# Kernel tuning notes

Measured on AMD Instinct MI355X. Metric: run time of the kernel, lower is better.

The kernel has to match this reference:

```python
import jax, jax.numpy as jnp
import numpy as np

E = 16        # extra_first_dim / num_experts
N = 32768     # total tokens (sum of num_inputs_per_group)
D = 2048      # input_dim
O = 2048      # output_dim


def setup_inputs() -> dict:
    key = jax.random.key(0)
    k1, k2 = jax.random.split(key)
    x = jax.random.normal(k1, (N, D), dtype=jnp.float32)
    weight = jax.random.normal(k2, (E, D, O), dtype=jnp.float32) * (1.0 / np.sqrt(D))
    # contiguous, equal-size groups summing to N (2048 tokens per expert)
    num_inputs_per_group = jnp.full((E,), N // E, dtype=jnp.int32)
    return {"x": x, "weight": weight, "num_inputs_per_group": num_inputs_per_group}


def reference(x, weight, num_inputs_per_group):
    # Grouped GEMM: rows of x are contiguous per group; row i uses weight[seg[i]].
    # seg: (N,) expert id per token, derived from group sizes (matches torch cumsum slicing).
    n_groups = weight.shape[0]
    n_tokens = x.shape[0]
    seg = jnp.repeat(jnp.arange(n_groups, dtype=jnp.int32), num_inputs_per_group,
                     total_repeat_length=n_tokens)

    def step(acc, ew):
        e, w = ew  # w: (D, O)
        xe = jnp.where((seg == e)[:, None], x, jnp.zeros((), x.dtype))  # mask rows of this group
        return acc + xe @ w, None

    init = jnp.zeros((n_tokens, weight.shape[2]), dtype=x.dtype)
    out, _ = jax.lax.scan(step, init, (jnp.arange(n_groups, dtype=jnp.int32), weight))
    # gang.size == 1: scatter_input / reduce_output are identities.
    return out
```

## Files before the change

### kernel.cpp

```cpp
#include <hip/hip_runtime.h>
#include <hip/hip_bf16.h>
#include <stdint.h>

#define N_TOK 32768
#define DIM   2048
#define ODIM  2048
#define NEXP  16

#define BM 256
#define BN 256
#define BK 64
#define NT (DIM / BK)

#define GLOBAL_AS __attribute__((address_space(1)))
#define LDS_AS    __attribute__((address_space(3)))

typedef short bf8_t  __attribute__((ext_vector_type(8)));
typedef float f4_t   __attribute__((ext_vector_type(4)));

__device__ __forceinline__ uint16_t f32_to_bf16_rne(float f) {
    uint32_t u = __float_as_uint(f);
    uint32_t r = (u + 0x7FFFu + ((u >> 16) & 1u)) >> 16;
    return (uint16_t)r;
}

__global__ void cvt_x_kernel(const float* __restrict__ x,
                             uint16_t* __restrict__ xb, int n4) {
    int i = blockIdx.x * blockDim.x + threadIdx.x;
    if (i >= n4) return;
    float4 v = ((const float4*)x)[i];
    ushort4 o;
    o.x = f32_to_bf16_rne(v.x);
    o.y = f32_to_bf16_rne(v.y);
    o.z = f32_to_bf16_rne(v.z);
    o.w = f32_to_bf16_rne(v.w);
    ((ushort4*)xb)[i] = o;
}

__global__ void cvt_wT_kernel(const float* __restrict__ w,
                              uint16_t* __restrict__ wT) {
    __shared__ float s[64][65];
    const int e  = blockIdx.z;
    const int o0 = blockIdx.x * 64;
    const int d0 = blockIdx.y * 64;
    const float*  we  = w  + (size_t)e * DIM * ODIM;
    uint16_t*     wTe = wT + (size_t)e * (size_t)ODIM * DIM;
    const int c  = threadIdx.x & 63;
    const int r0 = threadIdx.x >> 6;
#pragma unroll
    for (int r = r0; r < 64; r += 4)
        s[r][c] = we[(size_t)(d0 + r) * ODIM + (o0 + c)];
    __syncthreads();
#pragma unroll
    for (int r = r0; r < 64; r += 4)
        wTe[(size_t)(o0 + r) * DIM + (d0 + c)] = f32_to_bf16_rne(s[c][r]);
}

__device__ __forceinline__ void async_copy16(const uint16_t* g, uint16_t* l) {
    __builtin_amdgcn_global_load_lds((const GLOBAL_AS void*)g,
                                     (LDS_AS void*)l, 16, 0, 0);
}

#define STAGE_A(BUF, HALF, KT) do {                                           \
    const uint16_t* _g = aSrc + (size_t)(HALF) * 128 * DIM + (KT) * 64;       \
    uint16_t* _l = aDst + (BUF) * 16384 + (HALF) * 8192;                      \
    async_copy16(_g, _l);                                                     \
    async_copy16(_g + (size_t)64 * DIM, _l + 4096);                           \
} while (0)

#define STAGE_B(BUF, HALF, KT) do {                                           \
    const uint16_t* _g = bSrc + (size_t)(HALF) * 128 * DIM + (KT) * 64;       \
    uint16_t* _l = bDst + (BUF) * 16384 + (HALF) * 8192;                      \
    async_copy16(_g, _l);                                                     \
    async_copy16(_g + (size_t)64 * DIM, _l + 4096);                           \
} while (0)

#define PHASE(BUF, MH, NH, STAGE_CODE, TAIL_CODE) do {                        \
    bf8_t af[4][2], bf[2][2];                                                 \
    const uint16_t* _a = Afr + (BUF) * 16384 + (MH) * 8192;                   \
    const uint16_t* _b = Bfr + (BUF) * 16384 + (NH) * 8192;                   \
    _Pragma("unroll") for (int mi = 0; mi < 4; ++mi)                          \
        _Pragma("unroll") for (int ks = 0; ks < 2; ++ks)                      \
            af[mi][ks] = *(const bf8_t*)(_a + mi * 1024 + ks * 32);           \
    _Pragma("unroll") for (int ni = 0; ni < 2; ++ni)                          \
        _Pragma("unroll") for (int ks = 0; ks < 2; ++ks)                      \
            bf[ni][ks] = *(const bf8_t*)(_b + ni * 1024 + ks * 32);           \
    STAGE_CODE                                                                \
    __builtin_amdgcn_s_barrier();                                             \
    asm volatile("s_waitcnt lgkmcnt(0)" ::: "memory");                        \
    __builtin_amdgcn_sched_barrier(0);                                        \
    __builtin_amdgcn_s_setprio(1);                                            \
    _Pragma("unroll") for (int ks = 0; ks < 2; ++ks)                          \
        _Pragma("unroll") for (int mi = 0; mi < 4; ++mi)                      \
            _Pragma("unroll") for (int ni = 0; ni < 2; ++ni)                  \
                acc[MH][NH][mi][ni] = __builtin_amdgcn_mfma_f32_16x16x32_bf16(\
                    af[mi][ks], bf[ni][ks], acc[MH][NH][mi][ni], 0, 0, 0);    \
    __builtin_amdgcn_s_setprio(0);                                            \
    TAIL_CODE                                                                 \
    __builtin_amdgcn_s_barrier();                                             \
} while (0)

__global__ void __launch_bounds__(512, 2)
grouped_gemm_kernel(const uint16_t* __restrict__ A,
                    const uint16_t* __restrict__ BT,
                    const int* __restrict__ gsize,
                    float* __restrict__ C) {
    __shared__ __align__(16) uint16_t smem[65536];

    const int bid = blockIdx.x;
    const int wg  = (bid & 7) * 128 + (bid >> 3);
    const int tile_m = wg >> 3;
    const int tile_n = wg & 7;
    const int row0 = tile_m * BM;
    const int col0 = tile_n * BN;

    int e = 0, base = 0;
#pragma unroll
    for (int i = 0; i < NEXP; ++i) {
        int nx = base + gsize[i];
        if (row0 >= nx) { base = nx; e = i + 1; }
    }
    const uint16_t* Be = BT + (size_t)e * (size_t)ODIM * DIM;

    const int tid  = threadIdx.x;
    const int lane = tid & 63;
    const int wave = tid >> 6;
    const int wm   = wave >> 2;
    const int wn   = wave & 3;
    const int fr   = lane & 15;
    const int fq   = lane >> 4;

    const int d0   = wave * 1024 + lane * 16;
    const int l0   = d0 ^ (((d0 >> 9) & 1) << 5);
    const int srow = l0 >> 7;
    const int scol = (l0 & 127) >> 1;
    const uint16_t* aSrc = A  + (size_t)(row0 + srow) * DIM + scol;
    const uint16_t* bSrc = Be + (size_t)(col0 + srow) * DIM + scol;
    uint16_t* const aDst = smem + wave * 512;
    uint16_t* const bDst = smem + 32768 + wave * 512;

    const int xorel = ((fr >> 2) & 1) << 4;
    const uint16_t* const Afr = smem + (size_t)(wm * 64 + fr) * 64
                                     + ((fq * 8) ^ xorel);
    const uint16_t* const Bfr = smem + 32768 + (size_t)(wn * 32 + fr) * 64
                                     + ((fq * 8) ^ xorel);

    f4_t acc[2][2][4][2] = {};

    STAGE_A(0, 0, 0); STAGE_A(0, 1, 0); STAGE_B(0, 0, 0); STAGE_B(0, 1, 0);
    STAGE_A(1, 0, 1); STAGE_B(1, 0, 1);
    asm volatile("s_waitcnt vmcnt(4)" ::: "memory");
    __builtin_amdgcn_s_barrier();

#pragma unroll 1
    for (int j = 0; j < NT; j += 2) {
        PHASE(0, 0, 0, { STAGE_A(1, 1, j + 1); STAGE_B(1, 1, j + 1); }, {});
        PHASE(0, 0, 1, {}, {});
        PHASE(0, 1, 0, { if (j + 2 < NT) STAGE_A(0, 0, j + 2); }, {});
        PHASE(0, 1, 1, { if (j + 2 < NT) STAGE_B(0, 0, j + 2); },
              { if (j + 2 < NT) asm volatile("s_waitcnt vmcnt(4)" ::: "memory");
                else            asm volatile("s_waitcnt vmcnt(0)" ::: "memory"); });
        PHASE(1, 0, 0, { if (j + 2 < NT) { STAGE_A(0, 1, j + 2); STAGE_B(0, 1, j + 2); } }, {});
        PHASE(1, 0, 1, {}, {});
        PHASE(1, 1, 0, { if (j + 3 < NT) STAGE_A(1, 0, j + 3); }, {});
        PHASE(1, 1, 1, { if (j + 3 < NT) STAGE_B(1, 0, j + 3); },
              { if (j + 3 < NT) asm volatile("s_waitcnt vmcnt(4)" ::: "memory");
                else            asm volatile("s_waitcnt vmcnt(0)" ::: "memory"); });
    }

    float* Cb = C + (size_t)(row0 + wm * 64 + fq * 4) * ODIM
                  + (col0 + wn * 32 + fr);
#pragma unroll
    for (int mh = 0; mh < 2; ++mh)
#pragma unroll
        for (int nh = 0; nh < 2; ++nh)
#pragma unroll
            for (int mi = 0; mi < 4; ++mi)
#pragma unroll
                for (int ni = 0; ni < 2; ++ni)
#pragma unroll
                    for (int r = 0; r < 4; ++r)
                        Cb[(size_t)(mh * 128 + mi * 16 + r) * ODIM
                           + nh * 128 + ni * 16] = acc[mh][nh][mi][ni][r];
}

extern "C" void kernel_launch(void* const* d_in, const int* in_sizes, int n_in,
                              void* d_out, int out_size, void* d_ws, size_t ws_size,
                              hipStream_t stream) {
    const float* x  = (const float*)d_in[0];
    const float* w  = (const float*)d_in[1];
    const int*   gs = (const int*)d_in[2];
    float* out = (float*)d_out;

    uint16_t* xb = (uint16_t*)d_ws;
    uint16_t* wT = xb + (size_t)N_TOK * DIM;

    int n4 = N_TOK * DIM / 4;
    cvt_x_kernel<<<(n4 + 255) / 256, 256, 0, stream>>>(x, xb, n4);

    dim3 tg(ODIM / 64, DIM / 64, NEXP);
    cvt_wT_kernel<<<tg, 256, 0, stream>>>(w, wT);

    grouped_gemm_kernel<<<dim3((ODIM / BN) * (N_TOK / BM)), 512, 0, stream>>>(
        xb, wT, gs, out);
}
```

Before: 948.6 us.

## Vectorize conversion kernels, reuse LDS fragments across phases, widen LDS swizzle

```diff
diff --git a/kernel.cpp b/kernel.cpp
--- a/kernel.cpp
+++ b/kernel.cpp
@@ -17,6 +17,7 @@
 
 typedef short bf8_t  __attribute__((ext_vector_type(8)));
 typedef float f4_t   __attribute__((ext_vector_type(4)));
+typedef unsigned short us8_t __attribute__((ext_vector_type(8)));
 
 __device__ __forceinline__ uint16_t f32_to_bf16_rne(float f) {
     uint32_t u = __float_as_uint(f);
@@ -25,16 +26,18 @@
 }
 
 __global__ void cvt_x_kernel(const float* __restrict__ x,
-                             uint16_t* __restrict__ xb, int n4) {
-    int i = blockIdx.x * blockDim.x + threadIdx.x;
-    if (i >= n4) return;
-    float4 v = ((const float4*)x)[i];
-    ushort4 o;
-    o.x = f32_to_bf16_rne(v.x);
-    o.y = f32_to_bf16_rne(v.y);
-    o.z = f32_to_bf16_rne(v.z);
-    o.w = f32_to_bf16_rne(v.w);
-    ((ushort4*)xb)[i] = o;
+                             uint16_t* __restrict__ xb, int n8) {
+    const int stride = gridDim.x * blockDim.x;
+    for (int i = blockIdx.x * blockDim.x + threadIdx.x; i < n8; i += stride) {
+        float4 a = ((const float4*)x)[2 * i];
+        float4 b = ((const float4*)x)[2 * i + 1];
+        us8_t o;
+        o[0] = f32_to_bf16_rne(a.x); o[1] = f32_to_bf16_rne(a.y);
+        o[2] = f32_to_bf16_rne(a.z); o[3] = f32_to_bf16_rne(a.w);
+        o[4] = f32_to_bf16_rne(b.x); o[5] = f32_to_bf16_rne(b.y);
+        o[6] = f32_to_bf16_rne(b.z); o[7] = f32_to_bf16_rne(b.w);
+        ((us8_t*)xb)[i] = o;
+    }
 }
 
 __global__ void cvt_wT_kernel(const float* __restrict__ w,
@@ -45,15 +48,24 @@
     const int d0 = blockIdx.y * 64;
     const float*  we  = w  + (size_t)e * DIM * ODIM;
     uint16_t*     wTe = wT + (size_t)e * (size_t)ODIM * DIM;
-    const int c  = threadIdx.x & 63;
-    const int r0 = threadIdx.x >> 6;
-#pragma unroll
-    for (int r = r0; r < 64; r += 4)
-        s[r][c] = we[(size_t)(d0 + r) * ODIM + (o0 + c)];
+    const int tid = threadIdx.x;
+    const int c4  = (tid & 15) * 4;
+    const int r0  = tid >> 4;
+#pragma unroll
+    for (int r = r0; r < 64; r += 16)
+        *(float4*)&s[r][c4] =
+            *(const float4*)&we[(size_t)(d0 + r) * ODIM + o0 + c4];
     __syncthreads();
-#pragma unroll
-    for (int r = r0; r < 64; r += 4)
-        wTe[(size_t)(o0 + r) * DIM + (d0 + c)] = f32_to_bf16_rne(s[c][r]);
+    const int g   = tid & 7;
+    const int or0 = tid >> 3;
+#pragma unroll
+    for (int oo = or0; oo < 64; oo += 32) {
+        us8_t v;
+#pragma unroll
+        for (int j = 0; j < 8; ++j)
+            v[j] = f32_to_bf16_rne(s[g * 8 + j][oo]);
+        *(us8_t*)&wTe[(size_t)(o0 + oo) * DIM + d0 + g * 8] = v;
+    }
 }
 
 __device__ __forceinline__ void async_copy16(const uint16_t* g, uint16_t* l) {
@@ -75,16 +87,25 @@
     async_copy16(_g + (size_t)64 * DIM, _l + 4096);                           \
 } while (0)
 
-#define PHASE(BUF, MH, NH, STAGE_CODE, TAIL_CODE) do {                        \
-    bf8_t af[4][2], bf[2][2];                                                 \
-    const uint16_t* _a = Afr + (BUF) * 16384 + (MH) * 8192;                   \
-    const uint16_t* _b = Bfr + (BUF) * 16384 + (NH) * 8192;                   \
-    _Pragma("unroll") for (int mi = 0; mi < 4; ++mi)                          \
-        _Pragma("unroll") for (int ks = 0; ks < 2; ++ks)                      \
-            af[mi][ks] = *(const bf8_t*)(_a + mi * 1024 + ks * 32);           \
-    _Pragma("unroll") for (int ni = 0; ni < 2; ++ni)                          \
-        _Pragma("unroll") for (int ks = 0; ks < 2; ++ks)                      \
-            bf[ni][ks] = *(const bf8_t*)(_b + ni * 1024 + ks * 32);           \
+#define LOAD_A(dst, BUF, MH) do {                                             \
+    const uint16_t* _p = smem + (BUF) * 16384 + (MH) * 8192;                  \
+    _Pragma("unroll") for (int mi = 0; mi < 4; ++mi) {                        \
+        const uint16_t* _r = _p + (wm * 64 + mi * 16 + fr) * 64;              \
+        dst[mi][0] = *(const bf8_t*)(_r + colk0);                             \
+        dst[mi][1] = *(const bf8_t*)(_r + colk1);                             \
+    }                                                                         \
+} while (0)
+
+#define LOAD_B(dst, BUF, NH) do {                                             \
+    const uint16_t* _p = smem + 32768 + (BUF) * 16384 + (NH) * 8192;          \
+    _Pragma("unroll") for (int ni = 0; ni < 2; ++ni) {                        \
+        const uint16_t* _r = _p + (wn * 32 + ni * 16 + fr) * 64;              \
+        dst[ni][0] = *(const bf8_t*)(_r + colk0);                             \
+        dst[ni][1] = *(const bf8_t*)(_r + colk1);                             \
+    }                                                                         \
+} while (0)
+
+#define PHASE_CORE(AF, BF, MH, NH, STAGE_CODE, TAIL_CODE) do {                \
     STAGE_CODE                                                                \
     __builtin_amdgcn_s_barrier();                                             \
     asm volatile("s_waitcnt lgkmcnt(0)" ::: "memory");                        \
@@ -94,7 +115,7 @@
         _Pragma("unroll") for (int mi = 0; mi < 4; ++mi)                      \
             _Pragma("unroll") for (int ni = 0; ni < 2; ++ni)                  \
                 acc[MH][NH][mi][ni] = __builtin_amdgcn_mfma_f32_16x16x32_bf16(\
-                    af[mi][ks], bf[ni][ks], acc[MH][NH][mi][ni], 0, 0, 0);    \
+                    AF[mi][ks], BF[ni][ks], acc[MH][NH][mi][ni], 0, 0, 0);    \
     __builtin_amdgcn_s_setprio(0);                                            \
     TAIL_CODE                                                                 \
     __builtin_amdgcn_s_barrier();                                             \
@@ -130,8 +151,8 @@
     const int fr   = lane & 15;
     const int fq   = lane >> 4;
 
-    const int d0   = wave * 1024 + lane * 16;
-    const int l0   = d0 ^ (((d0 >> 9) & 1) << 5);
+    const int d0b = wave * 1024 + lane * 16;
+    const int l0  = d0b ^ (((d0b >> 9) & 1) << 5) ^ (((d0b >> 10) & 1) << 6);
     const int srow = l0 >> 7;
     const int scol = (l0 & 127) >> 1;
     const uint16_t* aSrc = A  + (size_t)(row0 + srow) * DIM + scol;
@@ -139,11 +160,9 @@
     uint16_t* const aDst = smem + wave * 512;
     uint16_t* const bDst = smem + 32768 + wave * 512;
 
-    const int xorel = ((fr >> 2) & 1) << 4;
-    const uint16_t* const Afr = smem + (size_t)(wm * 64 + fr) * 64
-                                     + ((fq * 8) ^ xorel);
-    const uint16_t* const Bfr = smem + 32768 + (size_t)(wn * 32 + fr) * 64
-                                     + ((fq * 8) ^ xorel);
+    const int xorel = (fr & 12) << 2;
+    const int colk0 = (fq * 8) ^ xorel;
+    const int colk1 = (fq * 8 + 32) ^ xorel;
 
     f4_t acc[2][2][4][2] = {};
 
@@ -154,16 +173,25 @@
 
 #pragma unroll 1
     for (int j = 0; j < NT; j += 2) {
-        PHASE(0, 0, 0, { STAGE_A(1, 1, j + 1); STAGE_B(1, 1, j + 1); }, {});
-        PHASE(0, 0, 1, {}, {});
-        PHASE(0, 1, 0, { if (j + 2 < NT) STAGE_A(0, 0, j + 2); }, {});
-        PHASE(0, 1, 1, { if (j + 2 < NT) STAGE_B(0, 0, j + 2); },
+        bf8_t af0[4][2], af1[4][2], bf0[2][2], bf1[2][2];
+        LOAD_A(af0, 0, 0); LOAD_B(bf0, 0, 0);
+        PHASE_CORE(af0, bf0, 0, 0,
+                   { STAGE_A(1, 1, j + 1); STAGE_B(1, 1, j + 1); }, {});
+        LOAD_B(bf1, 0, 1);
+        PHASE_CORE(af0, bf1, 0, 1, {}, {});
+        LOAD_A(af1, 0, 1);
+        PHASE_CORE(af1, bf0, 1, 0, { if (j + 2 < NT) STAGE_A(0, 0, j + 2); }, {});
+        PHASE_CORE(af1, bf1, 1, 1, { if (j + 2 < NT) STAGE_B(0, 0, j + 2); },
               { if (j + 2 < NT) asm volatile("s_waitcnt vmcnt(4)" ::: "memory");
                 else            asm volatile("s_waitcnt vmcnt(0)" ::: "memory"); });
-        PHASE(1, 0, 0, { if (j + 2 < NT) { STAGE_A(0, 1, j + 2); STAGE_B(0, 1, j + 2); } }, {});
-        PHASE(1, 0, 1, {}, {});
-        PHASE(1, 1, 0, { if (j + 3 < NT) STAGE_A(1, 0, j + 3); }, {});
-        PHASE(1, 1, 1, { if (j + 3 < NT) STAGE_B(1, 0, j + 3); },
+        LOAD_A(af0, 1, 0); LOAD_B(bf0, 1, 0);
+        PHASE_CORE(af0, bf0, 0, 0,
+                   { if (j + 2 < NT) { STAGE_A(0, 1, j + 2); STAGE_B(0, 1, j + 2); } }, {});
+        LOAD_B(bf1, 1, 1);
+        PHASE_CORE(af0, bf1, 0, 1, {}, {});
+        LOAD_A(af1, 1, 1);
+        PHASE_CORE(af1, bf0, 1, 0, { if (j + 3 < NT) STAGE_A(1, 0, j + 3); }, {});
+        PHASE_CORE(af1, bf1, 1, 1, { if (j + 3 < NT) STAGE_B(1, 0, j + 3); },
               { if (j + 3 < NT) asm volatile("s_waitcnt vmcnt(4)" ::: "memory");
                 else            asm volatile("s_waitcnt vmcnt(0)" ::: "memory"); });
     }
@@ -195,8 +223,8 @@
     uint16_t* xb = (uint16_t*)d_ws;
     uint16_t* wT = xb + (size_t)N_TOK * DIM;
 
-    int n4 = N_TOK * DIM / 4;
-    cvt_x_kernel<<<(n4 + 255) / 256, 256, 0, stream>>>(x, xb, n4);
+    int n8 = N_TOK * DIM / 8;
+    cvt_x_kernel<<<4096, 256, 0, stream>>>(x, xb, n8);
 
     dim3 tg(ODIM / 64, DIM / 64, NEXP);
     cvt_wT_kernel<<<tg, 256, 0, stream>>>(w, wT);
```

Result: faster. 862.8 us (-9.0%).
